# Kernel optimization log

Measured on AMD Instinct MI355X. Metric: run time of the kernel, lower is better.

The kernel has to match this reference:

```python
import jax, jax.numpy as jnp
import numpy as np

KERNEL_SIZE = 11  # matches init kwarg
EPS = 1e-5       # denominator guard used by the CUDA kernel


def setup_inputs() -> dict:
    key = jax.random.key(0)
    k1, k2 = jax.random.split(key)
    B, C, H, W = 4, 3, 512, 512
    image = jax.random.uniform(k1, (B, C, H, W), dtype=jnp.float32)
    # per-pixel Gaussian sigma map in (0.3, 3.3)
    psf = jax.random.uniform(k2, (B, H, W), dtype=jnp.float32) * 3.0 + 0.3
    return {"image": image, "psf": psf}


def _gauss_psf(image, psf, kernel_size):
    # image: [B,C,H,W]; psf: [B,C,H,W] per-pixel sigma.
    # Gather form: out[p] = sum_q img[q] * k(q) / sum_q k(q),
    # k(q) = exp(-(dx^2+dy^2) / (2*sigma[q]^2 + eps)), q in KxK window,
    # out-of-image neighbors skipped (validity mask).
    r = kernel_size // 2
    H, W = image.shape[-2], image.shape[-1]
    pad = ((0, 0), (0, 0), (r, r), (r, r))
    img_p = jnp.pad(image, pad)
    w_p = jnp.pad(psf, pad)
    m_p = jnp.pad(jnp.ones_like(psf), pad)  # validity mask
    out = jnp.zeros_like(image)
    wsum = jnp.zeros_like(image)
    for dy in range(kernel_size):      # loop over fixed kernel offsets, not data dims
        for dx in range(kernel_size):
            d2 = float((dy - r) ** 2 + (dx - r) ** 2)
            iv = img_p[..., dy:dy + H, dx:dx + W]
            wv = w_p[..., dy:dy + H, dx:dx + W]
            mv = m_p[..., dy:dy + H, dx:dx + W]
            k = mv * jnp.exp(-d2 / (2.0 * wv * wv + EPS))
            out = out + iv * k
            wsum = wsum + k
    return out / wsum  # center tap contributes k=1, so wsum >= 1


def reference(image, psf):
    # psf.unsqueeze(1).expand_as(image): broadcast sigma map over channels
    psf_bc = jnp.broadcast_to(psf[:, None, :, :], image.shape)
    return _gauss_psf(image, psf_bc, KERNEL_SIZE)
```

## Files before the change

### kernel.cpp

```cpp
#include <hip/hip_runtime.h>

#define HH 512
#define WW 512
#define HW (HH * WW)
#define RR 5
#define KS 11
#define EPS_F 1e-5f
#define NLOG2E 1.44269504088896340736f
#define TW 64
#define TH 4
#define BY 5
#define SW (TW + 2 * RR)
#define SH (TH + 2 * RR)
#define NSTRIP (SW * TH)
#define NT (SH * SW)

typedef float f2 __attribute__((ext_vector_type(2)));
__device__ __forceinline__ f2 fma2(f2 a, f2 b, f2 c) { return __builtin_elementwise_fma(a, b, c); }

__global__ __launch_bounds__(320) void gauss_psf_kernel(const float* __restrict__ image,
                                                        const float* __restrict__ psf,
                                                        float* __restrict__ out) {
    __shared__ float4 sm[6 * NSTRIP];

    const int tx  = threadIdx.x;
    const int ty  = threadIdx.y;
    const int tid = ty * 64 + tx;
    const int bx0 = blockIdx.x * TW;
    const int by0 = blockIdx.y * TH;
    const int b   = blockIdx.z;

    const float* pw   = psf + (size_t)b * HW;
    const float* img0 = image + (size_t)b * 3 * HW;

#pragma unroll
    for (int base = 0; base < NT; base += 320) {
        const int idx = base + tid;
        if (idx < NT) {
            const int row = idx / SW, col = idx - row * SW;
            const int gy = by0 - RR + row, gx = bx0 - RR + col;
            const bool in = ((unsigned)gy < (unsigned)HH) && ((unsigned)gx < (unsigned)WW);
            const int cy = gy < 0 ? 0 : (gy > HH - 1 ? HH - 1 : gy);
            const int cx = gx < 0 ? 0 : (gx > WW - 1 ? WW - 1 : gx);
            const int ni = cy * WW + cx;
            const float w  = pw[ni];
            const float i0 = img0[ni];
            const float i1 = img0[ni + HW];
            const float i2 = img0[ni + 2 * HW];
            const float a = -NLOG2E * __builtin_amdgcn_rcpf(fmaf(2.0f * w, w, EPS_F));
            const float t = in ? __builtin_amdgcn_exp2f(a) : 0.0f;
            sm[idx] = make_float4(t, i0, i1, i2);
        }
    }
    __syncthreads();

    f2 a0p[3], a1p[3], a2p[3], awp[3];
#pragma unroll
    for (int p = 0; p < 3; ++p) {
        a0p[p] = (f2)0.0f; a1p[p] = (f2)0.0f; a2p[p] = (f2)0.0f; awp[p] = (f2)0.0f;
    }

    if (tid < NSTRIP) {
        const int ly = tid / SW;
        const int lx = tid - ly * SW;
        const int sidx = ly * SW + lx;

#pragma unroll
        for (int r = 0; r < KS; ++r) {
            const float4 v = sm[sidx + r * SW];
            const float t = v.x, i0 = v.y, i1 = v.z, i2 = v.w;

            const float t2 = t * t, t4 = t2 * t2, t8 = t4 * t4;
            const float t9 = t8 * t, t16 = t8 * t8, t25 = t16 * t9;

            const int ii = (r - RR) * (r - RR);
            const float u = ii == 0 ? 1.0f : ii == 1 ? t : ii == 4 ? t4
                          : ii == 9 ? t9 : ii == 16 ? t16 : t25;

            const f2 u2  = {u, u};
            const f2 f01 = u2 * (f2){1.0f, t};
            const f2 f23 = u2 * (f2){t4, t9};
            const f2 f45 = u2 * (f2){t16, t25};

            const f2 i0v = {i0, i0}, i1v = {i1, i1}, i2v = {i2, i2};
            a0p[0] = fma2(i0v, f01, a0p[0]);
            a0p[1] = fma2(i0v, f23, a0p[1]);
            a0p[2] = fma2(i0v, f45, a0p[2]);
            a1p[0] = fma2(i1v, f01, a1p[0]);
            a1p[1] = fma2(i1v, f23, a1p[1]);
            a1p[2] = fma2(i1v, f45, a1p[2]);
            a2p[0] = fma2(i2v, f01, a2p[0]);
            a2p[1] = fma2(i2v, f23, a2p[1]);
            a2p[2] = fma2(i2v, f45, a2p[2]);
            awp[0] += f01;
            awp[1] += f23;
            awp[2] += f45;
        }
    }
    __syncthreads();

    if (tid < NSTRIP) {
#pragma unroll
        for (int p = 0; p < 3; ++p) {
            sm[(2 * p) * NSTRIP + tid]     = make_float4(a0p[p].x, a1p[p].x, a2p[p].x, awp[p].x);
            sm[(2 * p + 1) * NSTRIP + tid] = make_float4(a0p[p].y, a1p[p].y, a2p[p].y, awp[p].y);
        }
    }
    __syncthreads();

    if (tid < TW * TH) {
        const int hx = tid & 63, hy = tid >> 6;
        const int hb = hy * SW + hx;
        f2 s01 = (f2)0.0f, s2w = (f2)0.0f;
#pragma unroll
        for (int j = 0; j < KS; ++j) {
            const int jj = (j - RR) * (j - RR);
            const int ai = jj == 0 ? 0 : jj == 1 ? 1 : jj == 4 ? 2
                         : jj == 9 ? 3 : jj == 16 ? 4 : 5;
            const float4 v = sm[ai * NSTRIP + hb + j];
            s01 += (f2){v.x, v.y};
            s2w += (f2){v.z, v.w};
        }

        const float sw = s2w.y;
        float inv = __builtin_amdgcn_rcpf(sw);
        inv = inv * (2.0f - sw * inv);
        const int x = bx0 + hx, y = by0 + hy;
        const int oi = y * WW + x;
        float* outb = out + (size_t)b * 3 * HW;
        outb[oi]          = s01.x * inv;
        outb[HW + oi]     = s01.y * inv;
        outb[2 * HW + oi] = s2w.x * inv;
    }
}

extern "C" void kernel_launch(void* const* d_in, const int* in_sizes, int n_in,
                              void* d_out, int out_size, void* d_ws, size_t ws_size,
                              hipStream_t stream) {
    const float* image = (const float*)d_in[0];
    const float* psf   = (const float*)d_in[1];
    float* out = (float*)d_out;

    dim3 block(TW, BY, 1);
    dim3 grid(WW / TW, HH / TH, 4);
    gauss_psf_kernel<<<grid, block, 0, stream>>>(image, psf, out);
}
```

Before: 84.54 us.

## Process four vertical tiles per block with a shared-memory ring buffer and prefetch

```diff
diff --git a/kernel.cpp b/kernel.cpp
--- a/kernel.cpp
+++ b/kernel.cpp
@@ -9,36 +9,40 @@
 #define NLOG2E 1.44269504088896340736f
 #define TW 64
 #define TH 4
+#define TPB 4
+#define CH (TH * TPB)
 #define BY 5
 #define SW (TW + 2 * RR)
 #define SH (TH + 2 * RR)
 #define NSTRIP (SW * TH)
-#define NT (SH * SW)
+#define RS 16
+#define PRO (SW * SH)
 
 typedef float f2 __attribute__((ext_vector_type(2)));
 __device__ __forceinline__ f2 fma2(f2 a, f2 b, f2 c) { return __builtin_elementwise_fma(a, b, c); }
 
-__global__ __launch_bounds__(320) void gauss_psf_kernel(const float* __restrict__ image,
-                                                        const float* __restrict__ psf,
-                                                        float* __restrict__ out) {
-    __shared__ float4 sm[6 * NSTRIP];
+__global__ __launch_bounds__(320, 4) void gauss_psf_kernel(const float* __restrict__ image,
+                                                           const float* __restrict__ psf,
+                                                           float* __restrict__ out) {
+    __shared__ float4 ring[RS * SW];
+    __shared__ float4 cp[6 * NSTRIP];
 
     const int tx  = threadIdx.x;
     const int ty  = threadIdx.y;
     const int tid = ty * 64 + tx;
     const int bx0 = blockIdx.x * TW;
-    const int by0 = blockIdx.y * TH;
+    const int byc = blockIdx.y * CH;
     const int b   = blockIdx.z;
 
     const float* pw   = psf + (size_t)b * HW;
     const float* img0 = image + (size_t)b * 3 * HW;
 
 #pragma unroll
-    for (int base = 0; base < NT; base += 320) {
+    for (int base = 0; base < PRO; base += 320) {
         const int idx = base + tid;
-        if (idx < NT) {
+        if (idx < PRO) {
             const int row = idx / SW, col = idx - row * SW;
-            const int gy = by0 - RR + row, gx = bx0 - RR + col;
+            const int gy = byc - RR + row, gx = bx0 - RR + col;
             const bool in = ((unsigned)gy < (unsigned)HH) && ((unsigned)gx < (unsigned)WW);
             const int cy = gy < 0 ? 0 : (gy > HH - 1 ? HH - 1 : gy);
             const int cx = gx < 0 ? 0 : (gx > WW - 1 ? WW - 1 : gx);
@@ -49,88 +53,115 @@
             const float i2 = img0[ni + 2 * HW];
             const float a = -NLOG2E * __builtin_amdgcn_rcpf(fmaf(2.0f * w, w, EPS_F));
             const float t = in ? __builtin_amdgcn_exp2f(a) : 0.0f;
-            sm[idx] = make_float4(t, i0, i1, i2);
+            ring[row * SW + col] = make_float4(t, i0, i1, i2);
         }
     }
     __syncthreads();
 
-    f2 a0p[3], a1p[3], a2p[3], awp[3];
-#pragma unroll
-    for (int p = 0; p < 3; ++p) {
-        a0p[p] = (f2)0.0f; a1p[p] = (f2)0.0f; a2p[p] = (f2)0.0f; awp[p] = (f2)0.0f;
-    }
-
-    if (tid < NSTRIP) {
-        const int ly = tid / SW;
-        const int lx = tid - ly * SW;
-        const int sidx = ly * SW + lx;
+    const int ly = tid / SW;
+    const int lx = tid - ly * SW;
+    const int gxs = bx0 - RR + lx;
+    const int cxs = gxs < 0 ? 0 : (gxs > WW - 1 ? WW - 1 : gxs);
+    const bool xin = (unsigned)gxs < (unsigned)WW;
 
 #pragma unroll
-        for (int r = 0; r < KS; ++r) {
-            const float4 v = sm[sidx + r * SW];
-            const float t = v.x, i0 = v.y, i1 = v.z, i2 = v.w;
+    for (int k = 0; k < TPB; ++k) {
+        const int y0 = byc + TH * k;
 
-            const float t2 = t * t, t4 = t2 * t2, t8 = t4 * t4;
-            const float t9 = t8 * t, t16 = t8 * t8, t25 = t16 * t9;
+        float sw_ = 0.0f, s0 = 0.0f, s1 = 0.0f, s2 = 0.0f;
+        bool stin = false;
+        if (k < TPB - 1 && tid < NSTRIP) {
+            const int gy = y0 + TH + RR + ly;
+            const int cy = gy > HH - 1 ? HH - 1 : gy;
+            const int ni = cy * WW + cxs;
+            sw_ = pw[ni];
+            s0  = img0[ni];
+            s1  = img0[ni + HW];
+            s2  = img0[ni + 2 * HW];
+            stin = (gy < HH) && xin;
+        }
 
-            const int ii = (r - RR) * (r - RR);
-            const float u = ii == 0 ? 1.0f : ii == 1 ? t : ii == 4 ? t4
-                          : ii == 9 ? t9 : ii == 16 ? t16 : t25;
-
-            const f2 u2  = {u, u};
-            const f2 f01 = u2 * (f2){1.0f, t};
-            const f2 f23 = u2 * (f2){t4, t9};
-            const f2 f45 = u2 * (f2){t16, t25};
-
-            const f2 i0v = {i0, i0}, i1v = {i1, i1}, i2v = {i2, i2};
-            a0p[0] = fma2(i0v, f01, a0p[0]);
-            a0p[1] = fma2(i0v, f23, a0p[1]);
-            a0p[2] = fma2(i0v, f45, a0p[2]);
-            a1p[0] = fma2(i1v, f01, a1p[0]);
-            a1p[1] = fma2(i1v, f23, a1p[1]);
-            a1p[2] = fma2(i1v, f45, a1p[2]);
-            a2p[0] = fma2(i2v, f01, a2p[0]);
-            a2p[1] = fma2(i2v, f23, a2p[1]);
-            a2p[2] = fma2(i2v, f45, a2p[2]);
-            awp[0] += f01;
-            awp[1] += f23;
-            awp[2] += f45;
-        }
-    }
-    __syncthreads();
-
-    if (tid < NSTRIP) {
+        f2 a0p[3], a1p[3], a2p[3], awp[3];
 #pragma unroll
         for (int p = 0; p < 3; ++p) {
-            sm[(2 * p) * NSTRIP + tid]     = make_float4(a0p[p].x, a1p[p].x, a2p[p].x, awp[p].x);
-            sm[(2 * p + 1) * NSTRIP + tid] = make_float4(a0p[p].y, a1p[p].y, a2p[p].y, awp[p].y);
-        }
-    }
-    __syncthreads();
-
-    if (tid < TW * TH) {
-        const int hx = tid & 63, hy = tid >> 6;
-        const int hb = hy * SW + hx;
-        f2 s01 = (f2)0.0f, s2w = (f2)0.0f;
-#pragma unroll
-        for (int j = 0; j < KS; ++j) {
-            const int jj = (j - RR) * (j - RR);
-            const int ai = jj == 0 ? 0 : jj == 1 ? 1 : jj == 4 ? 2
-                         : jj == 9 ? 3 : jj == 16 ? 4 : 5;
-            const float4 v = sm[ai * NSTRIP + hb + j];
-            s01 += (f2){v.x, v.y};
-            s2w += (f2){v.z, v.w};
+            a0p[p] = (f2)0.0f; a1p[p] = (f2)0.0f; a2p[p] = (f2)0.0f; awp[p] = (f2)0.0f;
         }
 
-        const float sw = s2w.y;
-        float inv = __builtin_amdgcn_rcpf(sw);
-        inv = inv * (2.0f - sw * inv);
-        const int x = bx0 + hx, y = by0 + hy;
-        const int oi = y * WW + x;
-        float* outb = out + (size_t)b * 3 * HW;
-        outb[oi]          = s01.x * inv;
-        outb[HW + oi]     = s01.y * inv;
-        outb[2 * HW + oi] = s2w.x * inv;
+        if (tid < NSTRIP) {
+#pragma unroll
+            for (int r = 0; r < KS; ++r) {
+                const int slot = (TH * k + ly + r) & (RS - 1);
+                const float4 v = ring[slot * SW + lx];
+                const float t = v.x, i0 = v.y, i1 = v.z, i2 = v.w;
+
+                const float t2 = t * t, t4 = t2 * t2, t8 = t4 * t4;
+                const float t9 = t8 * t, t16 = t8 * t8, t25 = t16 * t9;
+
+                const int ii = (r - RR) * (r - RR);
+                const float u = ii == 0 ? 1.0f : ii == 1 ? t : ii == 4 ? t4
+                              : ii == 9 ? t9 : ii == 16 ? t16 : t25;
+
+                const f2 u2  = {u, u};
+                const f2 f01 = u2 * (f2){1.0f, t};
+                const f2 f23 = u2 * (f2){t4, t9};
+                const f2 f45 = u2 * (f2){t16, t25};
+
+                const f2 i0v = {i0, i0}, i1v = {i1, i1}, i2v = {i2, i2};
+                a0p[0] = fma2(i0v, f01, a0p[0]);
+                a0p[1] = fma2(i0v, f23, a0p[1]);
+                a0p[2] = fma2(i0v, f45, a0p[2]);
+                a1p[0] = fma2(i1v, f01, a1p[0]);
+                a1p[1] = fma2(i1v, f23, a1p[1]);
+                a1p[2] = fma2(i1v, f45, a1p[2]);
+                a2p[0] = fma2(i2v, f01, a2p[0]);
+                a2p[1] = fma2(i2v, f23, a2p[1]);
+                a2p[2] = fma2(i2v, f45, a2p[2]);
+                awp[0] += f01;
+                awp[1] += f23;
+                awp[2] += f45;
+            }
+        }
+        __syncthreads();
+
+        if (k < TPB - 1 && tid < NSTRIP) {
+            const float a = -NLOG2E * __builtin_amdgcn_rcpf(fmaf(2.0f * sw_, sw_, EPS_F));
+            const float t = stin ? __builtin_amdgcn_exp2f(a) : 0.0f;
+            ring[((TH * k + SH + ly) & (RS - 1)) * SW + lx] = make_float4(t, s0, s1, s2);
+        }
+
+        if (tid < NSTRIP) {
+#pragma unroll
+            for (int p = 0; p < 3; ++p) {
+                cp[(2 * p) * NSTRIP + tid]     = make_float4(a0p[p].x, a1p[p].x, a2p[p].x, awp[p].x);
+                cp[(2 * p + 1) * NSTRIP + tid] = make_float4(a0p[p].y, a1p[p].y, a2p[p].y, awp[p].y);
+            }
+        }
+        __syncthreads();
+
+        if (tid < TW * TH) {
+            const int hx = tid & 63, hy = tid >> 6;
+            const int hb = hy * SW + hx;
+            f2 s01 = (f2)0.0f, s2w = (f2)0.0f;
+#pragma unroll
+            for (int j = 0; j < KS; ++j) {
+                const int jj = (j - RR) * (j - RR);
+                const int ai = jj == 0 ? 0 : jj == 1 ? 1 : jj == 4 ? 2
+                             : jj == 9 ? 3 : jj == 16 ? 4 : 5;
+                const float4 v = cp[ai * NSTRIP + hb + j];
+                s01 += (f2){v.x, v.y};
+                s2w += (f2){v.z, v.w};
+            }
+
+            const float swv = s2w.y;
+            float inv = __builtin_amdgcn_rcpf(swv);
+            inv = inv * (2.0f - swv * inv);
+            const int x = bx0 + hx, y = y0 + hy;
+            const int oi = y * WW + x;
+            float* outb = out + (size_t)b * 3 * HW;
+            outb[oi]          = s01.x * inv;
+            outb[HW + oi]     = s01.y * inv;
+            outb[2 * HW + oi] = s2w.x * inv;
+        }
     }
 }
 
@@ -142,6 +173,6 @@
     float* out = (float*)d_out;
 
     dim3 block(TW, BY, 1);
-    dim3 grid(WW / TW, HH / TH, 4);
+    dim3 grid(WW / TW, HH / CH, 4);
     gauss_psf_kernel<<<grid, block, 0, stream>>>(image, psf, out);
 }
```

Measured after the change: 94.30 us. 1.12x slower.

## Replace shared-memory tile staging with per-wave direct global column loads

Applied to the files above, without the earlier changes.

```diff
diff --git a/kernel.cpp b/kernel.cpp
--- a/kernel.cpp
+++ b/kernel.cpp
@@ -7,52 +7,30 @@
 #define KS 11
 #define EPS_F 1e-5f
 #define NLOG2E 1.44269504088896340736f
-#define TW 64
-#define TH 4
-#define BY 5
-#define SW (TW + 2 * RR)
-#define SH (TH + 2 * RR)
-#define NSTRIP (SW * TH)
-#define NT (SH * SW)
+#define OPW 54
+#define NG 10
 
 typedef float f2 __attribute__((ext_vector_type(2)));
 __device__ __forceinline__ f2 fma2(f2 a, f2 b, f2 c) { return __builtin_elementwise_fma(a, b, c); }
 
-__global__ __launch_bounds__(320) void gauss_psf_kernel(const float* __restrict__ image,
-                                                        const float* __restrict__ psf,
-                                                        float* __restrict__ out) {
-    __shared__ float4 sm[6 * NSTRIP];
+__global__ __launch_bounds__(256, 6) void gauss_psf_kernel(const float* __restrict__ image,
+                                                           const float* __restrict__ psf,
+                                                           float* __restrict__ out) {
+    __shared__ float4 smH[4][6][64];
 
-    const int tx  = threadIdx.x;
-    const int ty  = threadIdx.y;
-    const int tid = ty * 64 + tx;
-    const int bx0 = blockIdx.x * TW;
-    const int by0 = blockIdx.y * TH;
-    const int b   = blockIdx.z;
+    const int lane = threadIdx.x;
+    const int ty   = threadIdx.y;
+    const int g    = blockIdx.x;
+    const int y    = blockIdx.y * 4 + ty;
+    const int b    = blockIdx.z;
+
+    const int c0   = (g == NG - 1) ? (WW - OPW) : g * OPW;
+    const int col  = c0 - RR + lane;
+    const int colc = col < 0 ? 0 : (col > WW - 1 ? WW - 1 : col);
+    const float xm = ((unsigned)col < (unsigned)WW) ? 1.0f : 0.0f;
 
     const float* pw   = psf + (size_t)b * HW;
     const float* img0 = image + (size_t)b * 3 * HW;
-
-#pragma unroll
-    for (int base = 0; base < NT; base += 320) {
-        const int idx = base + tid;
-        if (idx < NT) {
-            const int row = idx / SW, col = idx - row * SW;
-            const int gy = by0 - RR + row, gx = bx0 - RR + col;
-            const bool in = ((unsigned)gy < (unsigned)HH) && ((unsigned)gx < (unsigned)WW);
-            const int cy = gy < 0 ? 0 : (gy > HH - 1 ? HH - 1 : gy);
-            const int cx = gx < 0 ? 0 : (gx > WW - 1 ? WW - 1 : gx);
-            const int ni = cy * WW + cx;
-            const float w  = pw[ni];
-            const float i0 = img0[ni];
-            const float i1 = img0[ni + HW];
-            const float i2 = img0[ni + 2 * HW];
-            const float a = -NLOG2E * __builtin_amdgcn_rcpf(fmaf(2.0f * w, w, EPS_F));
-            const float t = in ? __builtin_amdgcn_exp2f(a) : 0.0f;
-            sm[idx] = make_float4(t, i0, i1, i2);
-        }
-    }
-    __syncthreads();
 
     f2 a0p[3], a1p[3], a2p[3], awp[3];
 #pragma unroll
@@ -60,73 +38,88 @@
         a0p[p] = (f2)0.0f; a1p[p] = (f2)0.0f; a2p[p] = (f2)0.0f; awp[p] = (f2)0.0f;
     }
 
-    if (tid < NSTRIP) {
-        const int ly = tid / SW;
-        const int lx = tid - ly * SW;
-        const int sidx = ly * SW + lx;
+    auto tap = [&](int r, float t, float i0, float i1, float i2) {
+        const float t2 = t * t, t4 = t2 * t2, t8 = t4 * t4;
+        const float t9 = t8 * t, t16 = t8 * t8, t25 = t16 * t9;
+
+        const int ii = (r - RR) * (r - RR);
+        const float u = ii == 0 ? 1.0f : ii == 1 ? t : ii == 4 ? t4
+                      : ii == 9 ? t9 : ii == 16 ? t16 : t25;
+
+        const f2 u2  = {u, u};
+        const f2 f01 = u2 * (f2){1.0f, t};
+        const f2 f23 = u2 * (f2){t4, t9};
+        const f2 f45 = u2 * (f2){t16, t25};
+
+        const f2 i0v = {i0, i0}, i1v = {i1, i1}, i2v = {i2, i2};
+        a0p[0] = fma2(i0v, f01, a0p[0]);
+        a0p[1] = fma2(i0v, f23, a0p[1]);
+        a0p[2] = fma2(i0v, f45, a0p[2]);
+        a1p[0] = fma2(i1v, f01, a1p[0]);
+        a1p[1] = fma2(i1v, f23, a1p[1]);
+        a1p[2] = fma2(i1v, f45, a1p[2]);
+        a2p[0] = fma2(i2v, f01, a2p[0]);
+        a2p[1] = fma2(i2v, f23, a2p[1]);
+        a2p[2] = fma2(i2v, f45, a2p[2]);
+        awp[0] += f01;
+        awp[1] += f23;
+        awp[2] += f45;
+    };
+
+    if (blockIdx.y >= 2 && blockIdx.y <= 125) {
+        const float* pb = img0 + (size_t)(y - RR) * WW + colc;
+        const float* wb = pw + (size_t)(y - RR) * WW + colc;
+#pragma unroll
+        for (int r = 0; r < KS; ++r) {
+            const float w  = wb[r * WW];
+            const float i0 = pb[r * WW];
+            const float i1 = pb[r * WW + HW];
+            const float i2 = pb[r * WW + 2 * HW];
+            const float a = -NLOG2E * __builtin_amdgcn_rcpf(fmaf(2.0f * w, w, EPS_F));
+            const float t = xm * __builtin_amdgcn_exp2f(a);
+            tap(r, t, i0, i1, i2);
+        }
+    } else {
+#pragma unroll
+        for (int r = 0; r < KS; ++r) {
+            const int gy = y - RR + r;
+            const int ry = gy < 0 ? 0 : (gy > HH - 1 ? HH - 1 : gy);
+            const float ym = ((unsigned)gy < (unsigned)HH) ? 1.0f : 0.0f;
+            const int ni = ry * WW + colc;
+            const float w  = pw[ni];
+            const float i0 = img0[ni];
+            const float i1 = img0[ni + HW];
+            const float i2 = img0[ni + 2 * HW];
+            const float a = -NLOG2E * __builtin_amdgcn_rcpf(fmaf(2.0f * w, w, EPS_F));
+            const float t = xm * ym * __builtin_amdgcn_exp2f(a);
+            tap(r, t, i0, i1, i2);
+        }
+    }
 
 #pragma unroll
-        for (int r = 0; r < KS; ++r) {
-            const float4 v = sm[sidx + r * SW];
-            const float t = v.x, i0 = v.y, i1 = v.z, i2 = v.w;
+    for (int p = 0; p < 3; ++p) {
+        smH[ty][2 * p][lane]     = make_float4(a0p[p].x, a1p[p].x, a2p[p].x, awp[p].x);
+        smH[ty][2 * p + 1][lane] = make_float4(a0p[p].y, a1p[p].y, a2p[p].y, awp[p].y);
+    }
 
-            const float t2 = t * t, t4 = t2 * t2, t8 = t4 * t4;
-            const float t9 = t8 * t, t16 = t8 * t8, t25 = t16 * t9;
+    const int lm = lane - RR;
+    const int lb = lm < 0 ? 0 : (lm > OPW - 1 ? OPW - 1 : lm);
+    f2 s01 = (f2)0.0f, s2w = (f2)0.0f;
+#pragma unroll
+    for (int j = 0; j < KS; ++j) {
+        const int jj = (j - RR) * (j - RR);
+        const int ai = jj == 0 ? 0 : jj == 1 ? 1 : jj == 4 ? 2
+                     : jj == 9 ? 3 : jj == 16 ? 4 : 5;
+        const float4 v = smH[ty][ai][lb + j];
+        s01 += (f2){v.x, v.y};
+        s2w += (f2){v.z, v.w};
+    }
 
-            const int ii = (r - RR) * (r - RR);
-            const float u = ii == 0 ? 1.0f : ii == 1 ? t : ii == 4 ? t4
-                          : ii == 9 ? t9 : ii == 16 ? t16 : t25;
-
-            const f2 u2  = {u, u};
-            const f2 f01 = u2 * (f2){1.0f, t};
-            const f2 f23 = u2 * (f2){t4, t9};
-            const f2 f45 = u2 * (f2){t16, t25};
-
-            const f2 i0v = {i0, i0}, i1v = {i1, i1}, i2v = {i2, i2};
-            a0p[0] = fma2(i0v, f01, a0p[0]);
-            a0p[1] = fma2(i0v, f23, a0p[1]);
-            a0p[2] = fma2(i0v, f45, a0p[2]);
-            a1p[0] = fma2(i1v, f01, a1p[0]);
-            a1p[1] = fma2(i1v, f23, a1p[1]);
-            a1p[2] = fma2(i1v, f45, a1p[2]);
-            a2p[0] = fma2(i2v, f01, a2p[0]);
-            a2p[1] = fma2(i2v, f23, a2p[1]);
-            a2p[2] = fma2(i2v, f45, a2p[2]);
-            awp[0] += f01;
-            awp[1] += f23;
-            awp[2] += f45;
-        }
-    }
-    __syncthreads();
-
-    if (tid < NSTRIP) {
-#pragma unroll
-        for (int p = 0; p < 3; ++p) {
-            sm[(2 * p) * NSTRIP + tid]     = make_float4(a0p[p].x, a1p[p].x, a2p[p].x, awp[p].x);
-            sm[(2 * p + 1) * NSTRIP + tid] = make_float4(a0p[p].y, a1p[p].y, a2p[p].y, awp[p].y);
-        }
-    }
-    __syncthreads();
-
-    if (tid < TW * TH) {
-        const int hx = tid & 63, hy = tid >> 6;
-        const int hb = hy * SW + hx;
-        f2 s01 = (f2)0.0f, s2w = (f2)0.0f;
-#pragma unroll
-        for (int j = 0; j < KS; ++j) {
-            const int jj = (j - RR) * (j - RR);
-            const int ai = jj == 0 ? 0 : jj == 1 ? 1 : jj == 4 ? 2
-                         : jj == 9 ? 3 : jj == 16 ? 4 : 5;
-            const float4 v = sm[ai * NSTRIP + hb + j];
-            s01 += (f2){v.x, v.y};
-            s2w += (f2){v.z, v.w};
-        }
-
-        const float sw = s2w.y;
-        float inv = __builtin_amdgcn_rcpf(sw);
-        inv = inv * (2.0f - sw * inv);
-        const int x = bx0 + hx, y = by0 + hy;
-        const int oi = y * WW + x;
+    if ((unsigned)lm < OPW) {
+        const float swv = s2w.y;
+        float inv = __builtin_amdgcn_rcpf(swv);
+        inv = inv * (2.0f - swv * inv);
+        const int oi = y * WW + col;
         float* outb = out + (size_t)b * 3 * HW;
         outb[oi]          = s01.x * inv;
         outb[HW + oi]     = s01.y * inv;
@@ -141,7 +134,7 @@
     const float* psf   = (const float*)d_in[1];
     float* out = (float*)d_out;
 
-    dim3 block(TW, BY, 1);
-    dim3 grid(WW / TW, HH / TH, 4);
+    dim3 block(64, 4, 1);
+    dim3 grid(NG, HH / 4, 4);
     gauss_psf_kernel<<<grid, block, 0, stream>>>(image, psf, out);
 }
```

Result: no change. 83.33 us (-1.4%).
